# Kernel tuning notes

Hardware: AMD Instinct MI355X
Metric: run time of the kernel (lower is better)

## Reference

```python
import jax, jax.numpy as jnp
import numpy as np

P = 0.5
SCALE_TRUE = 10.0
SCALE_WRONG = -10.0
B, C = 2048, 50257


def setup_inputs() -> dict:
    key = jax.random.key(0)
    k1, k2 = jax.random.split(key)
    output = jax.random.normal(k1, (B, C), dtype=jnp.float32)
    labels = jax.random.randint(k2, (B,), 0, C, dtype=jnp.int64)
    return {"output": output, "labels": labels}


def reference(output, labels):
    b, c = output.shape
    rows = jnp.arange(b)

    # tempOut: positive logits scaled by scale_wrong, else 0
    temp_out = jnp.where(output > 0, output * SCALE_WRONG, jnp.zeros_like(output))

    # tempLabels: filled with scale_wrong; target entry per row set to
    # max(|mean(row)|, |row[label]|) * scale_true
    gathered = output[rows, labels]                     # [B]
    row_val = jnp.maximum(jnp.abs(jnp.mean(output, axis=1)), jnp.abs(gathered)) * SCALE_TRUE
    temp_labels = jnp.full_like(output, SCALE_WRONG).at[rows, labels].set(row_val)

    # L1 loss (mean reduction over all elements)
    l1 = jnp.mean(jnp.abs(temp_out - temp_labels))

    # Cross-entropy (mean over batch)
    log_probs = jax.nn.log_softmax(output, axis=1)      # [B, C]
    ce = -jnp.mean(log_probs[rows, labels])

    return P * l1 + (1.0 - P) * ce
```

## Files before the change

### kernel.cpp

```cpp
#include <hip/hip_runtime.h>
#include <hip/hip_bf16.h>
#include <stdint.h>

#define BATCH 2048
#define NCLS  50257
#define LOG2E 1.44269504088896340736f
#define LN2   0.69314718055994530942f

typedef float v4f __attribute__((ext_vector_type(4)));

__device__ __forceinline__ float l1_base(float v) {
    return fabsf(1.f - fmaxf(v, 0.f));
}

__global__ __launch_bounds__(256) void custom_loss_kernel(
    const float* __restrict__ x,
    const int*   __restrict__ labels,
    float*       __restrict__ result)
{
    const int row = blockIdx.x;
    const int tid = threadIdx.x;
    const float* rp = x + (size_t)row * NCLS;

    float sum0 = 0.f, sum1 = 0.f;
    float l10  = 0.f, l11  = 0.f;
    float es0  = 0.f, es1  = 0.f;

    const int peel_full = (int)(((16u - ((uintptr_t)rp & 15u)) & 15u) >> 2);
    const int peel = peel_full > NCLS ? NCLS : peel_full;
    if (tid < peel) {
        float v = rp[tid];
        sum0 += v;
        l10  += l1_base(v);
        es0  += exp2f(v * LOG2E);
    }

    const v4f* rp4 = (const v4f*)(rp + peel);
    const int n4 = (NCLS - peel) >> 2;
    int i = tid;
    for (; i + 256 < n4; i += 512) {
        v4f a = __builtin_nontemporal_load(&rp4[i]);
        v4f b = __builtin_nontemporal_load(&rp4[i + 256]);

        sum0 += (a.x + a.y) + (a.z + a.w);
        sum1 += (b.x + b.y) + (b.z + b.w);

        l10 += (l1_base(a.x) + l1_base(a.y)) + (l1_base(a.z) + l1_base(a.w));
        l11 += (l1_base(b.x) + l1_base(b.y)) + (l1_base(b.z) + l1_base(b.w));

        es0 += (exp2f(a.x * LOG2E) + exp2f(a.y * LOG2E))
             + (exp2f(a.z * LOG2E) + exp2f(a.w * LOG2E));
        es1 += (exp2f(b.x * LOG2E) + exp2f(b.y * LOG2E))
             + (exp2f(b.z * LOG2E) + exp2f(b.w * LOG2E));
    }
    for (; i < n4; i += 256) {
        v4f a = __builtin_nontemporal_load(&rp4[i]);
        sum0 += (a.x + a.y) + (a.z + a.w);
        l10  += (l1_base(a.x) + l1_base(a.y)) + (l1_base(a.z) + l1_base(a.w));
        es0  += (exp2f(a.x * LOG2E) + exp2f(a.y * LOG2E))
              + (exp2f(a.z * LOG2E) + exp2f(a.w * LOG2E));
    }

    const int tail = peel + (n4 << 2);
    for (int j = tail + tid; j < NCLS; j += 256) {
        float v = rp[j];
        sum0 += v;
        l10  += l1_base(v);
        es0  += exp2f(v * LOG2E);
    }

    float sum_x = sum0 + sum1;
    float l1b   = l10 + l11;
    float es    = es0 + es1;

    #pragma unroll
    for (int off = 32; off > 0; off >>= 1) {
        sum_x += __shfl_down(sum_x, off);
        l1b   += __shfl_down(l1b,   off);
        es    += __shfl_down(es,    off);
    }

    __shared__ float red[3][4];
    const int lane = tid & 63, wave = tid >> 6;
    if (lane == 0) { red[0][wave] = sum_x; red[1][wave] = l1b; red[2][wave] = es; }
    __syncthreads();

    if (tid == 0) {
        float S = 0.f, L = 0.f, E = 0.f;
        #pragma unroll
        for (int w = 0; w < 4; ++w) { S += red[0][w]; L += red[1][w]; E += red[2][w]; }

        const int   label = labels[row];
        const float g     = rp[label];

        const float mean    = S * (1.f / (float)NCLS);
        const float row_val = fmaxf(fabsf(mean), fabsf(g)) * 10.f;
        const float tout_g  = (g > 0.f) ? -10.f * g : 0.f;
        const float base_g  = 10.f * l1_base(g);
        const float l1_row  = 10.f * L - base_g + fabsf(tout_g - row_val);

        const float ce_row  = __log2f(E) * LN2 - g;

        const float inv_bc = 1.f / ((float)BATCH * (float)NCLS);
        const float inv_b  = 1.f / (float)BATCH;
        const float contrib = 0.5f * l1_row * inv_bc + 0.5f * ce_row * inv_b;
        atomicAdd(result, contrib);
    }
}

extern "C" void kernel_launch(void* const* d_in, const int* in_sizes, int n_in,
                              void* d_out, int out_size, void* d_ws, size_t ws_size,
                              hipStream_t stream) {
    const float* x      = (const float*)d_in[0];
    const int*   labels = (const int*)d_in[1];
    float*       out    = (float*)d_out;

    (void)hipMemsetAsync(out, 0, sizeof(float), stream);

    custom_loss_kernel<<<BATCH, 256, 0, stream>>>(x, labels, out);
}
```

Before: 517.6 us.

## Unroll row loop 4x, drop nontemporal loads, replace atomic with workspace reduction

Unrolls the per-thread streaming loop from two to four independent float4 loads with separate accumulators, so more memory requests are in flight per thread. Switches from nontemporal loads to ordinary loads and adds a launch-bounds occupancy hint. When a workspace is available, each row writes its contribution to a buffer and a second single-block kernel sums them, replacing the memset plus global atomicAdd. This adds a kernel launch and raises register pressure.

```diff
diff --git a/kernel.cpp b/kernel.cpp
--- a/kernel.cpp
+++ b/kernel.cpp
@@ -1,5 +1,4 @@
 #include <hip/hip_runtime.h>
-#include <hip/hip_bf16.h>
 #include <stdint.h>
 
 #define BATCH 2048
@@ -13,98 +12,127 @@
     return fabsf(1.f - fmaxf(v, 0.f));
 }
 
-__global__ __launch_bounds__(256) void custom_loss_kernel(
+template<bool USE_WS>
+__global__ __launch_bounds__(256, 4) void custom_loss_kernel(
     const float* __restrict__ x,
     const int*   __restrict__ labels,
-    float*       __restrict__ result)
+    float*       __restrict__ out)
 {
     const int row = blockIdx.x;
     const int tid = threadIdx.x;
     const float* rp = x + (size_t)row * NCLS;
 
-    float sum0 = 0.f, sum1 = 0.f;
-    float l10  = 0.f, l11  = 0.f;
-    float es0  = 0.f, es1  = 0.f;
+    float s0=0.f, s1=0.f, s2=0.f, s3=0.f;
+    float a0=0.f, a1=0.f, a2=0.f, a3=0.f;
+    float e0=0.f, e1=0.f, e2=0.f, e3=0.f;
 
     const int peel_full = (int)(((16u - ((uintptr_t)rp & 15u)) & 15u) >> 2);
     const int peel = peel_full > NCLS ? NCLS : peel_full;
     if (tid < peel) {
         float v = rp[tid];
-        sum0 += v;
-        l10  += l1_base(v);
-        es0  += exp2f(v * LOG2E);
+        s0 += v; a0 += l1_base(v); e0 += exp2f(v * LOG2E);
     }
 
     const v4f* rp4 = (const v4f*)(rp + peel);
     const int n4 = (NCLS - peel) >> 2;
     int i = tid;
-    for (; i + 256 < n4; i += 512) {
-        v4f a = __builtin_nontemporal_load(&rp4[i]);
-        v4f b = __builtin_nontemporal_load(&rp4[i + 256]);
+    for (; i + 768 < n4; i += 1024) {
+        v4f a = rp4[i];
+        v4f b = rp4[i + 256];
+        v4f c = rp4[i + 512];
+        v4f d = rp4[i + 768];
 
-        sum0 += (a.x + a.y) + (a.z + a.w);
-        sum1 += (b.x + b.y) + (b.z + b.w);
+        s0 += (a.x + a.y) + (a.z + a.w);
+        s1 += (b.x + b.y) + (b.z + b.w);
+        s2 += (c.x + c.y) + (c.z + c.w);
+        s3 += (d.x + d.y) + (d.z + d.w);
 
-        l10 += (l1_base(a.x) + l1_base(a.y)) + (l1_base(a.z) + l1_base(a.w));
-        l11 += (l1_base(b.x) + l1_base(b.y)) + (l1_base(b.z) + l1_base(b.w));
+        a0 += (l1_base(a.x) + l1_base(a.y)) + (l1_base(a.z) + l1_base(a.w));
+        a1 += (l1_base(b.x) + l1_base(b.y)) + (l1_base(b.z) + l1_base(b.w));
+        a2 += (l1_base(c.x) + l1_base(c.y)) + (l1_base(c.z) + l1_base(c.w));
+        a3 += (l1_base(d.x) + l1_base(d.y)) + (l1_base(d.z) + l1_base(d.w));
 
-        es0 += (exp2f(a.x * LOG2E) + exp2f(a.y * LOG2E))
-             + (exp2f(a.z * LOG2E) + exp2f(a.w * LOG2E));
-        es1 += (exp2f(b.x * LOG2E) + exp2f(b.y * LOG2E))
-             + (exp2f(b.z * LOG2E) + exp2f(b.w * LOG2E));
+        e0 += (exp2f(a.x * LOG2E) + exp2f(a.y * LOG2E))
+            + (exp2f(a.z * LOG2E) + exp2f(a.w * LOG2E));
+        e1 += (exp2f(b.x * LOG2E) + exp2f(b.y * LOG2E))
+            + (exp2f(b.z * LOG2E) + exp2f(b.w * LOG2E));
+        e2 += (exp2f(c.x * LOG2E) + exp2f(c.y * LOG2E))
+            + (exp2f(c.z * LOG2E) + exp2f(c.w * LOG2E));
+        e3 += (exp2f(d.x * LOG2E) + exp2f(d.y * LOG2E))
+            + (exp2f(d.z * LOG2E) + exp2f(d.w * LOG2E));
     }
     for (; i < n4; i += 256) {
-        v4f a = __builtin_nontemporal_load(&rp4[i]);
-        sum0 += (a.x + a.y) + (a.z + a.w);
-        l10  += (l1_base(a.x) + l1_base(a.y)) + (l1_base(a.z) + l1_base(a.w));
-        es0  += (exp2f(a.x * LOG2E) + exp2f(a.y * LOG2E))
-              + (exp2f(a.z * LOG2E) + exp2f(a.w * LOG2E));
+        v4f a = rp4[i];
+        s0 += (a.x + a.y) + (a.z + a.w);
+        a0 += (l1_base(a.x) + l1_base(a.y)) + (l1_base(a.z) + l1_base(a.w));
+        e0 += (exp2f(a.x * LOG2E) + exp2f(a.y * LOG2E))
+            + (exp2f(a.z * LOG2E) + exp2f(a.w * LOG2E));
     }
 
     const int tail = peel + (n4 << 2);
     for (int j = tail + tid; j < NCLS; j += 256) {
         float v = rp[j];
-        sum0 += v;
-        l10  += l1_base(v);
-        es0  += exp2f(v * LOG2E);
+        s0 += v; a0 += l1_base(v); e0 += exp2f(v * LOG2E);
     }
 
-    float sum_x = sum0 + sum1;
-    float l1b   = l10 + l11;
-    float es    = es0 + es1;
+    float S = (s0 + s1) + (s2 + s3);
+    float L = (a0 + a1) + (a2 + a3);
+    float E = (e0 + e1) + (e2 + e3);
 
     #pragma unroll
     for (int off = 32; off > 0; off >>= 1) {
-        sum_x += __shfl_down(sum_x, off);
-        l1b   += __shfl_down(l1b,   off);
-        es    += __shfl_down(es,    off);
+        S += __shfl_down(S, off);
+        L += __shfl_down(L, off);
+        E += __shfl_down(E, off);
     }
 
     __shared__ float red[3][4];
     const int lane = tid & 63, wave = tid >> 6;
-    if (lane == 0) { red[0][wave] = sum_x; red[1][wave] = l1b; red[2][wave] = es; }
+    if (lane == 0) { red[0][wave] = S; red[1][wave] = L; red[2][wave] = E; }
     __syncthreads();
 
     if (tid == 0) {
-        float S = 0.f, L = 0.f, E = 0.f;
-        #pragma unroll
-        for (int w = 0; w < 4; ++w) { S += red[0][w]; L += red[1][w]; E += red[2][w]; }
+        float Sa = (red[0][0] + red[0][1]) + (red[0][2] + red[0][3]);
+        float La = (red[1][0] + red[1][1]) + (red[1][2] + red[1][3]);
+        float Ea = (red[2][0] + red[2][1]) + (red[2][2] + red[2][3]);
 
         const int   label = labels[row];
         const float g     = rp[label];
 
-        const float mean    = S * (1.f / (float)NCLS);
+        const float mean    = Sa * (1.f / (float)NCLS);
         const float row_val = fmaxf(fabsf(mean), fabsf(g)) * 10.f;
         const float tout_g  = (g > 0.f) ? -10.f * g : 0.f;
-        const float base_g  = 10.f * l1_base(g);
-        const float l1_row  = 10.f * L - base_g + fabsf(tout_g - row_val);
+        const float l1_row  = 10.f * La - 10.f * l1_base(g) + fabsf(tout_g - row_val);
 
-        const float ce_row  = __log2f(E) * LN2 - g;
+        const float ce_row  = __log2f(Ea) * LN2 - g;
 
         const float inv_bc = 1.f / ((float)BATCH * (float)NCLS);
         const float inv_b  = 1.f / (float)BATCH;
         const float contrib = 0.5f * l1_row * inv_bc + 0.5f * ce_row * inv_b;
-        atomicAdd(result, contrib);
+
+        if (USE_WS) out[row] = contrib;
+        else        atomicAdd(out, contrib);
+    }
+}
+
+__global__ __launch_bounds__(1024) void reduce_rows_kernel(
+    const float* __restrict__ rc, float* __restrict__ result)
+{
+    const int tid = threadIdx.x;
+    float v = rc[tid] + rc[tid + 1024];
+    #pragma unroll
+    for (int off = 32; off > 0; off >>= 1) v += __shfl_down(v, off);
+
+    __shared__ float red[16];
+    const int lane = tid & 63, wave = tid >> 6;
+    if (lane == 0) red[wave] = v;
+    __syncthreads();
+
+    if (tid == 0) {
+        float t = 0.f;
+        #pragma unroll
+        for (int w = 0; w < 16; ++w) t += red[w];
+        *result = t;
     }
 }
 
@@ -115,7 +143,12 @@
     const int*   labels = (const int*)d_in[1];
     float*       out    = (float*)d_out;
 
-    (void)hipMemsetAsync(out, 0, sizeof(float), stream);
-
-    custom_loss_kernel<<<BATCH, 256, 0, stream>>>(x, labels, out);
+    if (d_ws && ws_size >= BATCH * sizeof(float)) {
+        float* rc = (float*)d_ws;
+        custom_loss_kernel<true><<<BATCH, 256, 0, stream>>>(x, labels, rc);
+        reduce_rows_kernel<<<1, 1024, 0, stream>>>(rc, out);
+    } else {
+        (void)hipMemsetAsync(out, 0, sizeof(float), stream);
+        custom_loss_kernel<false><<<BATCH, 256, 0, stream>>>(x, labels, out);
+    }
 }
```

After: 538.6 us. 4.1% more time.
